# Performance work log

Hardware: AMD Instinct MI355X
Metric: run time of the kernel (lower is better)

Reference implementation:

```python
import jax, jax.numpy as jnp
import numpy as np

B, C, N = 16, 256, 2048  # C = channels_m, inputs have C//2 channels
C2 = C // 2
BN_EPS = 1e-5


def setup_inputs() -> dict:
    key = jax.random.key(0)
    ks = jax.random.split(key, 8)
    s = 1.0 / np.sqrt(C2)
    return {
        "q": jax.random.normal(ks[0], (B, C2, N), dtype=jnp.float32),
        "x": jax.random.normal(ks[1], (B, C2, N), dtype=jnp.float32),
        "Wq": jax.random.normal(ks[2], (C2, C2), dtype=jnp.float32) * s,
        "Wk": jax.random.normal(ks[3], (C2, C2), dtype=jnp.float32) * s,
        "Wv": jax.random.normal(ks[4], (C, C2), dtype=jnp.float32) * s,
        "bv": jax.random.normal(ks[5], (C,), dtype=jnp.float32) * 0.01,
        "Wt": jax.random.normal(ks[6], (C, C), dtype=jnp.float32) * (1.0 / np.sqrt(C)),
        "bt": jax.random.normal(ks[7], (C,), dtype=jnp.float32) * 0.01,
        "gamma": jnp.ones((C,), dtype=jnp.float32),
        "beta": jnp.zeros((C,), dtype=jnp.float32),
        "running_mean": jnp.zeros((C,), dtype=jnp.float32),
        "running_var": jnp.ones((C,), dtype=jnp.float32),
    }


def reference(q, x, Wq, Wk, Wv, bv, Wt, bt, gamma, beta, running_mean, running_var):
    # 1x1 Conv1d == channel matmul. q, x: [B, C2, N]
    x_q = jnp.einsum('oc,bcn->bno', Wq, q)                     # [B, N, C2]
    x_k = jnp.einsum('oc,bcn->bon', Wk, x)                     # [B, C2, N]
    x_v = jnp.einsum('oc,bcn->bon', Wv, q) + bv[None, :, None]  # [B, C, N]

    energy = jnp.einsum('bnc,bcm->bnm', x_q, x_k)              # [B, N, N]
    attn = jax.nn.softmax(energy, axis=-1)
    # extra column-wise L1 renormalization (offset-attention)
    attn = attn / (1e-9 + attn.sum(axis=1, keepdims=True))

    x_r = jnp.einsum('bcn,bnm->bcm', x_v, attn)                # [B, C, N]
    x2 = jnp.einsum('oc,bcn->bon', Wv, x) + bv[None, :, None]  # v_conv(x): [B, C, N]

    t = jnp.einsum('oc,bcn->bon', Wt, x2 - x_r) + bt[None, :, None]
    inv = gamma * jax.lax.rsqrt(running_var + BN_EPS)
    bn = t * inv[None, :, None] + (beta - running_mean * inv)[None, :, None]
    return jax.nn.relu(bn) + x2
```

## Files before the change

kernel.cpp:

```cpp
#include <hip/hip_runtime.h>
#include <hip/hip_bf16.h>
#include <math.h>

#define BB 16
#define CC 256
#define C2 128
#define NN 2048

typedef __attribute__((ext_vector_type(8))) _Float16 f16x8;
typedef __attribute__((ext_vector_type(8))) short bf16x8;
typedef __attribute__((ext_vector_type(16))) float f32x16;
typedef unsigned short u16;

#define OFF_X2   ((size_t)0)
#define OFF_U16  ((size_t)16777216)
#define UOFF_XQT ((size_t)0)
#define UOFF_XKT ((size_t)4194304)
#define UOFF_XV  ((size_t)8388608)
#define OFF_RMAX ((size_t)25165824)
#define OFF_RSUM ((size_t)25198592)
#define OFF_W16  ((size_t)29458432)
#define WOFF_WQ  ((size_t)0)
#define WOFF_WK  ((size_t)16384)
#define WOFF_WV  ((size_t)32768)
#define WOFF_WT  ((size_t)65536)

__device__ __forceinline__ u16 f2h(float f) {
    union { _Float16 h; u16 u; } v; v.h = (_Float16)f;
    return v.u;
}
__device__ __forceinline__ u16 f2bf(float f) {
    union { float f; unsigned u; } v; v.f = f;
    return (u16)((v.u + 0x7fffu + ((v.u >> 16) & 1u)) >> 16);
}

__global__ __launch_bounds__(256) void prep_w(
    const float* __restrict__ Wq, const float* __restrict__ Wk,
    const float* __restrict__ Wv, const float* __restrict__ Wt,
    u16* __restrict__ w16)
{
    int i = blockIdx.x * 256 + threadIdx.x;
    float v; u16* dst; int o, c, KC;
    if (i < 16384)      { v = Wq[i]; o = i >> 7; c = i & 127; KC = 16; dst = w16; }
    else if (i < 32768) { int j = i - 16384; v = Wk[j]; o = j >> 7; c = j & 127; KC = 16; dst = w16 + 16384; }
    else if (i < 65536) { int j = i - 32768; v = Wv[j]; o = j >> 7; c = j & 127; KC = 16; dst = w16 + 32768; }
    else                { int j = i - 65536; v = Wt[j]; o = j >> 8; c = j & 255; KC = 32; dst = w16 + 65536; }
    int idx = (((o >> 5) * KC + (c >> 3)) << 8) + ((o & 31) << 3) + (c & 7);
    dst[idx] = f2h(v);
}

__global__ __launch_bounds__(256, 2) void proj_fused(
    const float* __restrict__ q, const float* __restrict__ x,
    const u16* __restrict__ wq16, const u16* __restrict__ wk16,
    const u16* __restrict__ wv16, const float* __restrict__ bias,
    u16* __restrict__ xqT, u16* __restrict__ xkT,
    u16* __restrict__ xv_bf, float* __restrict__ x2_f32)
{
    __shared__ u16 t_s[64 * 136];
    __shared__ u16 st[16384];
    int tid = threadIdx.x, lane = tid & 63, wave = tid >> 6;
    int zb = blockIdx.z, b = zb >> 1, which = zb & 1;
    int n0 = blockIdx.x * 64;
    const float* in  = which ? x : q;
    const u16*   wqk = which ? wk16 : wq16;
    u16*         outT = which ? xkT : xqT;
    {
        int r = tid >> 2;
        int nc = (tid & 3) * 16;
        #pragma unroll
        for (int hh = 0; hh < 2; ++hh) {
            const float4* ip4 = (const float4*)(in + ((size_t)b * C2 + hh * 64 + r) * NN + n0 + nc);
            #pragma unroll
            for (int jj = 0; jj < 4; ++jj) {
                float4 v = ip4[jj];
                int nbase = nc + jj * 4;
                t_s[(nbase + 0) * 136 + hh * 64 + r] = f2h(v.x);
                t_s[(nbase + 1) * 136 + hh * 64 + r] = f2h(v.y);
                t_s[(nbase + 2) * 136 + hh * 64 + r] = f2h(v.z);
                t_s[(nbase + 3) * 136 + hh * 64 + r] = f2h(v.w);
            }
        }
    }
    __syncthreads();
    int nsub = wave & 1, g = wave >> 1;
    int lrow = lane & 31, h = lane >> 5, lk8 = h * 8;
    const u16* brow = &t_s[(nsub * 32 + lrow) * 136 + lk8];
    f32x16 aq0, aq1, av0, av1, av2, av3;
    #pragma unroll
    for (int r = 0; r < 16; ++r)
        { aq0[r]=0.f; aq1[r]=0.f; av0[r]=0.f; av1[r]=0.f; av2[r]=0.f; av3[r]=0.f; }
    const u16* wqA = wqk  + (size_t)(2 * g) * 4096 + h * 256 + lrow * 8;
    const u16* wvA = wv16 + (size_t)(4 * g) * 4096 + h * 256 + lrow * 8;
    #pragma unroll
    for (int kk = 0; kk < 8; ++kk) {
        f16x8 bf = *(const f16x8*)&brow[kk * 16];
        f16x8 q0 = *(const f16x8*)&wqA[kk * 512];
        f16x8 q1 = *(const f16x8*)&wqA[4096 + kk * 512];
        aq0 = __builtin_amdgcn_mfma_f32_32x32x16_f16(bf, q0, aq0, 0, 0, 0);
        aq1 = __builtin_amdgcn_mfma_f32_32x32x16_f16(bf, q1, aq1, 0, 0, 0);
        f16x8 v0 = *(const f16x8*)&wvA[kk * 512];
        f16x8 v1 = *(const f16x8*)&wvA[4096 + kk * 512];
        f16x8 v2 = *(const f16x8*)&wvA[8192 + kk * 512];
        f16x8 v3 = *(const f16x8*)&wvA[12288 + kk * 512];
        av0 = __builtin_amdgcn_mfma_f32_32x32x16_f16(v0, bf, av0, 0, 0, 0);
        av1 = __builtin_amdgcn_mfma_f32_32x32x16_f16(v1, bf, av1, 0, 0, 0);
        av2 = __builtin_amdgcn_mfma_f32_32x32x16_f16(v2, bf, av2, 0, 0, 0);
        av3 = __builtin_amdgcn_mfma_f32_32x32x16_f16(v3, bf, av3, 0, 0, 0);
    }
    __syncthreads();
    {
        int off = (nsub * 16 + g * 8 + (lrow >> 3)) * 256 + (lrow & 7);
        #pragma unroll
        for (int r = 0; r < 16; ++r) {
            int ro = (r & 3) + 8 * (r >> 2) + 4 * h;
            t_s[off + ro * 8]        = f2h(aq0[r]);
            t_s[off + 1024 + ro * 8] = f2h(aq1[r]);
        }
    }
    if (which == 0) {
        int off = (g * 4 * 8 + nsub * 4 + (lrow >> 3)) * 256 + (lrow & 7);
        #pragma unroll
        for (int r = 0; r < 16; ++r) {
            int ro = (r & 3) + 8 * (r >> 2) + 4 * h;
            int c0r = g * 128 + ro;
            st[off + ro * 8]        = f2bf(av0[r] + bias[c0r]);
            st[off + 2048 + ro * 8] = f2bf(av1[r] + bias[c0r + 32]);
            st[off + 4096 + ro * 8] = f2bf(av2[r] + bias[c0r + 64]);
            st[off + 6144 + ro * 8] = f2bf(av3[r] + bias[c0r + 96]);
        }
    }
    __syncthreads();
    {
        u16* outb = outT + (size_t)b * NN * C2 + (size_t)(n0 >> 5) * 4096;
        for (int i = tid; i < 1024; i += 256)
            *(uint4*)&outb[i * 8] = *(uint4*)&t_s[i * 8];
    }
    if (which == 0) {
        u16* xvb = xv_bf + (size_t)b * CC * NN + (size_t)(n0 >> 3) * 256;
        for (int i = tid; i < 2048; i += 256) {
            int ct = i >> 8, j = i & 255;
            *(uint4*)&xvb[(size_t)ct * 65536 + j * 8] = *(uint4*)&st[ct * 2048 + j * 8];
        }
    } else {
        int n = n0 + nsub * 32 + lrow;
        #pragma unroll
        for (int r = 0; r < 16; ++r) {
            int ro = (r & 3) + 8 * (r >> 2) + 4 * h;
            int c0r = g * 128 + ro;
            x2_f32[((size_t)b * CC + c0r) * NN + n]      = av0[r] + bias[c0r];
            x2_f32[((size_t)b * CC + c0r + 32) * NN + n] = av1[r] + bias[c0r + 32];
            x2_f32[((size_t)b * CC + c0r + 64) * NN + n] = av2[r] + bias[c0r + 64];
            x2_f32[((size_t)b * CC + c0r + 96) * NN + n] = av3[r] + bias[c0r + 96];
        }
    }
}

__global__ __launch_bounds__(512, 4) void rowstats_mfma(
    const u16* __restrict__ xqT, const u16* __restrict__ xkT,
    float* __restrict__ rmax, float* __restrict__ rsum)
{
    __shared__ float Mp[8][32];
    __shared__ float Sp[8][32];
    const int tid  = threadIdx.x;
    int flat = blockIdx.x + gridDim.x * blockIdx.y;
    int xcd = flat & 7, rank = flat >> 3;
    const int b  = xcd * 2 + (rank >> 5);
    const int n0 = (rank & 31) * 64;
    const int lane = tid & 63;
    const int wave = tid >> 6;
    const int lrow = lane & 31;
    const int h    = lane >> 5;
    const u16* xqb = xqT + (size_t)b * NN * C2;
    const u16* xkb = xkT + (size_t)b * NN * C2;
    const int mquad = wave >> 1, nsub = wave & 1;

    f16x8 bR[8];
    {
        const u16* bp = xqb + ((size_t)((n0 >> 5) + nsub) * 16) * 256 + h * 256 + lrow * 8;
        #pragma unroll
        for (int kk = 0; kk < 8; ++kk) bR[kk] = *(const f16x8*)&bp[kk * 512];
    }
    float runM = -1e30f, runS = 0.f;
    const u16* ap = xkb + (size_t)(mquad * 16) * 256 + h * 256 + lrow * 8;
    for (int m0 = 0; m0 < NN; m0 += 128) {
        f32x16 e0;
        #pragma unroll
        for (int r = 0; r < 16; ++r) e0[r] = 0.f;
        #pragma unroll
        for (int kk = 0; kk < 8; ++kk) {
            f16x8 a0 = *(const f16x8*)&ap[kk * 512];
            e0 = __builtin_amdgcn_mfma_f32_32x32x16_f16(a0, bR[kk], e0, 0, 0, 0);
        }
        ap += 16384;
        float tm = e0[0];
        #pragma unroll
        for (int r = 1; r < 16; ++r) tm = fmaxf(tm, e0[r]);
        float newM = fmaxf(runM, tm);
        float sc = __expf(runM - newM);
        float ts = 0.f;
        #pragma unroll
        for (int r = 0; r < 16; ++r) ts += __expf(e0[r] - newM);
        runS = runS * sc + ts;
        runM = newM;
    }
    float oM = __shfl_xor(runM, 32, 64);
    float oS = __shfl_xor(runS, 32, 64);
    float M2 = fmaxf(runM, oM);
    float S2 = runS * __expf(runM - M2) + oS * __expf(oM - M2);
    if (lane < 32) { Mp[wave][lane] = M2; Sp[wave][lane] = S2; }
    __syncthreads();
    if (tid < 64) {
        int ns = tid >> 5, li = tid & 31;
        float Ma = Mp[ns][li],     Mb = Mp[ns + 2][li];
        float Mc = Mp[ns + 4][li], Md = Mp[ns + 6][li];
        float Mf = fmaxf(fmaxf(Ma, Mb), fmaxf(Mc, Md));
        float Sf = Sp[ns][li]     * __expf(Ma - Mf) + Sp[ns + 2][li] * __expf(Mb - Mf)
                 + Sp[ns + 4][li] * __expf(Mc - Mf) + Sp[ns + 6][li] * __expf(Md - Mf);
        rmax[(size_t)b * NN + n0 + tid] = Mf;
        rsum[(size_t)b * NN + n0 + tid] = Sf;
    }
}

__global__ __launch_bounds__(512, 4) void pv_mfma(
    const u16* __restrict__ xqT, const u16* __restrict__ xkT,
    const u16* __restrict__ xv, const float* __restrict__ rmax,
    const float* __restrict__ rsum, const float* __restrict__ x2,
    const u16* __restrict__ wt16, const float* __restrict__ bt,
    const float* __restrict__ gamma, const float* __restrict__ beta,
    const float* __restrict__ rmean, const float* __restrict__ rvar,
    float* __restrict__ out)
{
    __shared__ __align__(16) u16 smem[19584];
    const int tid = threadIdx.x;
    int flat = blockIdx.x + gridDim.x * blockIdx.y;
    int xcd = flat & 7, rank = flat >> 3;
    const int b  = xcd * 2 + (rank >> 5);
    const int m0 = (rank & 31) * 64;
    const int lane = tid & 63;
    const int wave = tid >> 6;
    const int lrow = lane & 31;
    const int h    = lane >> 5;
    const int lk8  = h * 8;
    const u16* xqb = xqT + (size_t)b * NN * C2;
    const u16* xkb = xkT + (size_t)b * NN * C2;
    const u16* xvb = xv  + (size_t)b * CC * NN;
    const float* rmx = rmax + (size_t)b * NN;
    const float* rsm = rsum + (size_t)b * NN;

    if (tid < 256) {
        float iv = gamma[tid] * rsqrtf(rvar[tid] + 1e-5f);
        float* bn = (float*)(smem + 18560);
        bn[tid]       = iv;
        bn[256 + tid] = bt[tid] * iv + beta[tid] - rmean[tid] * iv;
    }

    f16x8 aK[8];
    {
        const u16* kp = xkb + ((size_t)((m0 >> 5) + (wave & 1)) * 16) * 256 + h * 256 + lrow * 8;
        #pragma unroll
        for (int kk = 0; kk < 8; ++kk) aK[kk] = *(const f16x8*)&kp[kk * 512];
    }
    const int nq = wave >> 1;
    const int nl = nq * 32 + lrow;
    const int mbase = (wave & 1) * 32 + 4 * h;
    const u16* bqbase = xqb + (size_t)nq * 4096 + h * 256 + lrow * 8;
    const u16* avbase = xvb + (size_t)wave * 65536 + h * 256 + lrow * 8;

    f32x16 acc00, acc01;
    #pragma unroll
    for (int r = 0; r < 16; ++r) { acc00[r] = 0.f; acc01[r] = 0.f; }
    float s_reg = 0.f;
    __syncthreads();

    for (int ph = 0; ph <= 16; ++ph) {
        f16x8 bq[8];
        float Mn = 0.f, Sn = 1.f;
        if (ph < 16) {
            const u16* bqp = bqbase + (size_t)ph * 16384;
            #pragma unroll
            for (int kk = 0; kk < 8; ++kk) bq[kk] = *(const f16x8*)&bqp[kk * 512];
            Mn = rmx[ph * 128 + nl];
            Sn = rsm[ph * 128 + nl];
        }
        if (ph >= 1) {
            const int t = ph - 1;
            const u16* p_prev = smem + (t & 1) * 8704;
            const u16* avp = avbase + (size_t)t * 4096;
            {
                const uint4* prp = (const uint4*)&p_prev[(tid & 63) * 136 + (tid >> 6) * 16];
                uint4 v0 = prp[0], v1 = prp[1];
                unsigned wsv[8] = {v0.x, v0.y, v0.z, v0.w, v1.x, v1.y, v1.z, v1.w};
                float ss = 0.f;
                #pragma unroll
                for (int j = 0; j < 8; ++j) {
                    union { unsigned u; float f; } lo, hi;
                    lo.u = wsv[j] << 16;
                    hi.u = wsv[j] & 0xffff0000u;
                    ss += lo.f + hi.f;
                }
                s_reg += ss;
            }
            const u16* br0 = &p_prev[lrow * 136 + lk8];
            const u16* br1 = &p_prev[(32 + lrow) * 136 + lk8];
            __builtin_amdgcn_s_setprio(1);
            #pragma unroll
            for (int kk = 0; kk < 8; ++kk) {
                bf16x8 a0 = *(const bf16x8*)&avp[kk * 512];
                bf16x8 b0 = *(const bf16x8*)&br0[kk * 16];
                bf16x8 b1 = *(const bf16x8*)&br1[kk * 16];
                acc00 = __builtin_amdgcn_mfma_f32_32x32x16_bf16(a0, b0, acc00, 0, 0, 0);
                acc01 = __builtin_amdgcn_mfma_f32_32x32x16_bf16(a0, b1, acc01, 0, 0, 0);
            }
            __builtin_amdgcn_s_setprio(0);
        }
        if (ph < 16) {
            f32x16 e0;
            #pragma unroll
            for (int r = 0; r < 16; ++r) e0[r] = 0.f;
            __builtin_amdgcn_s_setprio(1);
            #pragma unroll
            for (int kk = 0; kk < 8; ++kk)
                e0 = __builtin_amdgcn_mfma_f32_32x32x16_f16(aK[kk], bq[kk], e0, 0, 0, 0);
            __builtin_amdgcn_s_setprio(0);
            float Si = 1.f / Sn;
            u16* p_cur = smem + (ph & 1) * 8704;
            #pragma unroll
            for (int r = 0; r < 16; ++r) {
                int ml = mbase + (r & 3) + 8 * (r >> 2);
                p_cur[ml * 136 + nl] = f2bf(__expf(e0[r] - Mn) * Si);
            }
        }
        __syncthreads();
    }
    float* s_part = (float*)(smem + 17408);
    s_part[(tid & 63) * 8 + (tid >> 6)] = s_reg;
    __syncthreads();
    float* sinv = (float*)(smem + 18432);
    if (tid < 64) {
        float ss = 0.f;
        #pragma unroll
        for (int j = 0; j < 8; ++j) ss += s_part[tid * 8 + j];
        sinv[tid] = 1.f / (1e-9f + ss);
    }
    __syncthreads();
    u16* dts = smem;
    const float* x2b = x2 + (size_t)b * CC * NN;
    float si0 = sinv[lrow], si1 = sinv[32 + lrow];
    #pragma unroll
    for (int r = 0; r < 16; ++r) {
        int ro = (r & 3) + 8 * (r >> 2) + 4 * h;
        int c = wave * 32 + ro;
        float d0 = x2b[(size_t)c * NN + m0 + lrow]      - acc00[r] * si0;
        float d1 = x2b[(size_t)c * NN + m0 + 32 + lrow] - acc01[r] * si1;
        dts[lrow * 264 + c]        = f2h(d0);
        dts[(32 + lrow) * 264 + c] = f2h(d1);
    }
    __syncthreads();
    {
        float* inv_s = (float*)(smem + 18560);
        float* add_s = inv_s + 256;
        int rt0 = (wave >> 1) * 2;
        int ns2 = wave & 1;
        const u16* brow2 = &dts[(ns2 * 32 + lrow) * 264 + lk8];
        const u16* a0p = wt16 + (size_t)rt0 * 8192 + h * 256 + lrow * 8;
        const u16* a1p = a0p + 8192;
        f32x16 o0a, o1a;
        #pragma unroll
        for (int r = 0; r < 16; ++r) { o0a[r] = 0.f; o1a[r] = 0.f; }
        #pragma unroll
        for (int kk = 0; kk < 16; ++kk) {
            f16x8 bb2 = *(const f16x8*)&brow2[kk * 16];
            f16x8 a0 = *(const f16x8*)&a0p[kk * 512];
            f16x8 a1 = *(const f16x8*)&a1p[kk * 512];
            o0a = __builtin_amdgcn_mfma_f32_32x32x16_f16(a0, bb2, o0a, 0, 0, 0);
            o1a = __builtin_amdgcn_mfma_f32_32x32x16_f16(a1, bb2, o1a, 0, 0, 0);
        }
        int n = m0 + ns2 * 32 + lrow;
        float* outb = out + (size_t)b * CC * NN;
        #pragma unroll
        for (int r = 0; r < 16; ++r) {
            int ro = (r & 3) + 8 * (r >> 2) + 4 * h;
            int ol0 = rt0 * 32 + ro, ol1 = ol0 + 32;
            float t0 = o0a[r] * inv_s[ol0] + add_s[ol0];
            float t1 = o1a[r] * inv_s[ol1] + add_s[ol1];
            outb[(size_t)ol0 * NN + n] = fmaxf(t0, 0.f) + x2b[(size_t)ol0 * NN + n];
            outb[(size_t)ol1 * NN + n] = fmaxf(t1, 0.f) + x2b[(size_t)ol1 * NN + n];
        }
    }
}

extern "C" void kernel_launch(void* const* d_in, const int* in_sizes, int n_in,
                              void* d_out, int out_size, void* d_ws, size_t ws_size,
                              hipStream_t stream)
{
    const float* q     = (const float*)d_in[0];
    const float* x     = (const float*)d_in[1];
    const float* Wq    = (const float*)d_in[2];
    const float* Wk    = (const float*)d_in[3];
    const float* Wv    = (const float*)d_in[4];
    const float* bv    = (const float*)d_in[5];
    const float* Wt    = (const float*)d_in[6];
    const float* bt    = (const float*)d_in[7];
    const float* gamma = (const float*)d_in[8];
    const float* beta  = (const float*)d_in[9];
    const float* rmean = (const float*)d_in[10];
    const float* rvar  = (const float*)d_in[11];
    float* out = (float*)d_out;
    float* ws  = (float*)d_ws;

    float* x2   = ws + OFF_X2;
    u16*   u1   = (u16*)(ws + OFF_U16);
    u16*   xqT  = u1 + UOFF_XQT;
    u16*   xkT  = u1 + UOFF_XKT;
    u16*   xv   = u1 + UOFF_XV;
    float* rmax = ws + OFF_RMAX;
    float* rsum = ws + OFF_RSUM;
    u16*   w16  = (u16*)(ws + OFF_W16);

    dim3 blk(256);
    prep_w<<<dim3(512), blk, 0, stream>>>(Wq, Wk, Wv, Wt, w16);
    proj_fused<<<dim3(NN/64, 1, 2*BB), blk, 0, stream>>>(
        q, x, w16 + WOFF_WQ, w16 + WOFF_WK, w16 + WOFF_WV, bv,
        xqT, xkT, xv, x2);
    rowstats_mfma<<<dim3(NN/64, BB), dim3(512), 0, stream>>>(xqT, xkT, rmax, rsum);
    pv_mfma<<<dim3(NN/64, BB), dim3(512), 0, stream>>>(
        xqT, xkT, xv, rmax, rsum, x2, w16 + WOFF_WT, bt, gamma, beta,
        rmean, rvar, out);
}
```

Before: 249.7 us.

## Drop weight prep kernel, convert fp32 weights inline; widen proj to 512 threads

Removes the separate prep_w launch that converted and tiled weights to fp16, and instead loads fp32 weights directly in the projection and output-transform MFMA loops, converting them to fp16 in registers. The projection kernel is also restructured to 512 threads per block with fewer accumulators per wave and a smaller staging buffer, writing xv in two staged passes. This saves one kernel launch and its global round trip. In exchange, each block reads fp32 weights at twice the bytes with strided row access and repeats the conversion work.

```diff
diff --git a/kernel.cpp b/kernel.cpp
--- a/kernel.cpp
+++ b/kernel.cpp
@@ -19,11 +19,6 @@
 #define UOFF_XV  ((size_t)8388608)
 #define OFF_RMAX ((size_t)25165824)
 #define OFF_RSUM ((size_t)25198592)
-#define OFF_W16  ((size_t)29458432)
-#define WOFF_WQ  ((size_t)0)
-#define WOFF_WK  ((size_t)16384)
-#define WOFF_WV  ((size_t)32768)
-#define WOFF_WT  ((size_t)65536)
 
 __device__ __forceinline__ u16 f2h(float f) {
     union { _Float16 h; u16 u; } v; v.h = (_Float16)f;
@@ -33,124 +28,112 @@
     union { float f; unsigned u; } v; v.f = f;
     return (u16)((v.u + 0x7fffu + ((v.u >> 16) & 1u)) >> 16);
 }
-
-__global__ __launch_bounds__(256) void prep_w(
+__device__ __forceinline__ f16x8 cvt8(const float* __restrict__ p) {
+    float4 a = *(const float4*)p;
+    float4 b = *(const float4*)(p + 4);
+    f16x8 r;
+    r[0] = (_Float16)a.x; r[1] = (_Float16)a.y;
+    r[2] = (_Float16)a.z; r[3] = (_Float16)a.w;
+    r[4] = (_Float16)b.x; r[5] = (_Float16)b.y;
+    r[6] = (_Float16)b.z; r[7] = (_Float16)b.w;
+    return r;
+}
+
+__global__ __launch_bounds__(512, 4) void proj_fused(
+    const float* __restrict__ q, const float* __restrict__ x,
     const float* __restrict__ Wq, const float* __restrict__ Wk,
-    const float* __restrict__ Wv, const float* __restrict__ Wt,
-    u16* __restrict__ w16)
-{
-    int i = blockIdx.x * 256 + threadIdx.x;
-    float v; u16* dst; int o, c, KC;
-    if (i < 16384)      { v = Wq[i]; o = i >> 7; c = i & 127; KC = 16; dst = w16; }
-    else if (i < 32768) { int j = i - 16384; v = Wk[j]; o = j >> 7; c = j & 127; KC = 16; dst = w16 + 16384; }
-    else if (i < 65536) { int j = i - 32768; v = Wv[j]; o = j >> 7; c = j & 127; KC = 16; dst = w16 + 32768; }
-    else                { int j = i - 65536; v = Wt[j]; o = j >> 8; c = j & 255; KC = 32; dst = w16 + 65536; }
-    int idx = (((o >> 5) * KC + (c >> 3)) << 8) + ((o & 31) << 3) + (c & 7);
-    dst[idx] = f2h(v);
-}
-
-__global__ __launch_bounds__(256, 2) void proj_fused(
-    const float* __restrict__ q, const float* __restrict__ x,
-    const u16* __restrict__ wq16, const u16* __restrict__ wk16,
-    const u16* __restrict__ wv16, const float* __restrict__ bias,
+    const float* __restrict__ Wv, const float* __restrict__ bias,
     u16* __restrict__ xqT, u16* __restrict__ xkT,
     u16* __restrict__ xv_bf, float* __restrict__ x2_f32)
 {
     __shared__ u16 t_s[64 * 136];
-    __shared__ u16 st[16384];
+    __shared__ u16 stg[8192];
     int tid = threadIdx.x, lane = tid & 63, wave = tid >> 6;
     int zb = blockIdx.z, b = zb >> 1, which = zb & 1;
     int n0 = blockIdx.x * 64;
     const float* in  = which ? x : q;
-    const u16*   wqk = which ? wk16 : wq16;
+    const float* wqk = which ? Wk : Wq;
     u16*         outT = which ? xkT : xqT;
     {
-        int r = tid >> 2;
-        int nc = (tid & 3) * 16;
-        #pragma unroll
-        for (int hh = 0; hh < 2; ++hh) {
-            const float4* ip4 = (const float4*)(in + ((size_t)b * C2 + hh * 64 + r) * NN + n0 + nc);
-            #pragma unroll
-            for (int jj = 0; jj < 4; ++jj) {
-                float4 v = ip4[jj];
-                int nbase = nc + jj * 4;
-                t_s[(nbase + 0) * 136 + hh * 64 + r] = f2h(v.x);
-                t_s[(nbase + 1) * 136 + hh * 64 + r] = f2h(v.y);
-                t_s[(nbase + 2) * 136 + hh * 64 + r] = f2h(v.z);
-                t_s[(nbase + 3) * 136 + hh * 64 + r] = f2h(v.w);
-            }
-        }
-    }
-    __syncthreads();
-    int nsub = wave & 1, g = wave >> 1;
+        int c  = tid >> 2;
+        int qn = (tid & 3) * 16;
+        const float4* ip4 = (const float4*)(in + ((size_t)b * C2 + c) * NN + n0 + qn);
+        #pragma unroll
+        for (int jj = 0; jj < 4; ++jj) {
+            float4 v = ip4[jj];
+            int nb = qn + jj * 4;
+            t_s[(nb + 0) * 136 + c] = f2h(v.x);
+            t_s[(nb + 1) * 136 + c] = f2h(v.y);
+            t_s[(nb + 2) * 136 + c] = f2h(v.z);
+            t_s[(nb + 3) * 136 + c] = f2h(v.w);
+        }
+    }
+    __syncthreads();
+    int nsub = wave & 1, gp = wave >> 1;
     int lrow = lane & 31, h = lane >> 5, lk8 = h * 8;
     const u16* brow = &t_s[(nsub * 32 + lrow) * 136 + lk8];
-    f32x16 aq0, aq1, av0, av1, av2, av3;
+    f32x16 aq0, av0, av1;
     #pragma unroll
-    for (int r = 0; r < 16; ++r)
-        { aq0[r]=0.f; aq1[r]=0.f; av0[r]=0.f; av1[r]=0.f; av2[r]=0.f; av3[r]=0.f; }
-    const u16* wqA = wqk  + (size_t)(2 * g) * 4096 + h * 256 + lrow * 8;
-    const u16* wvA = wv16 + (size_t)(4 * g) * 4096 + h * 256 + lrow * 8;
+    for (int r = 0; r < 16; ++r) { aq0[r] = 0.f; av0[r] = 0.f; av1[r] = 0.f; }
+    const float* wqA  = wqk + (size_t)(gp * 32 + lrow) * C2 + h * 8;
+    const float* wvA0 = Wv  + (size_t)(gp * 64 + lrow) * C2 + h * 8;
+    const float* wvA1 = Wv  + (size_t)(gp * 64 + 32 + lrow) * C2 + h * 8;
     #pragma unroll
     for (int kk = 0; kk < 8; ++kk) {
         f16x8 bf = *(const f16x8*)&brow[kk * 16];
-        f16x8 q0 = *(const f16x8*)&wqA[kk * 512];
-        f16x8 q1 = *(const f16x8*)&wqA[4096 + kk * 512];
+        f16x8 q0 = cvt8(&wqA[kk * 16]);
         aq0 = __builtin_amdgcn_mfma_f32_32x32x16_f16(bf, q0, aq0, 0, 0, 0);
-        aq1 = __builtin_amdgcn_mfma_f32_32x32x16_f16(bf, q1, aq1, 0, 0, 0);
-        f16x8 v0 = *(const f16x8*)&wvA[kk * 512];
-        f16x8 v1 = *(const f16x8*)&wvA[4096 + kk * 512];
-        f16x8 v2 = *(const f16x8*)&wvA[8192 + kk * 512];
-        f16x8 v3 = *(const f16x8*)&wvA[12288 + kk * 512];
+        f16x8 v0 = cvt8(&wvA0[kk * 16]);
+        f16x8 v1 = cvt8(&wvA1[kk * 16]);
         av0 = __builtin_amdgcn_mfma_f32_32x32x16_f16(v0, bf, av0, 0, 0, 0);
         av1 = __builtin_amdgcn_mfma_f32_32x32x16_f16(v1, bf, av1, 0, 0, 0);
-        av2 = __builtin_amdgcn_mfma_f32_32x32x16_f16(v2, bf, av2, 0, 0, 0);
-        av3 = __builtin_amdgcn_mfma_f32_32x32x16_f16(v3, bf, av3, 0, 0, 0);
-    }
-    __syncthreads();
-    {
-        int off = (nsub * 16 + g * 8 + (lrow >> 3)) * 256 + (lrow & 7);
+    }
+    {
+        int off = (nsub * 16 + gp * 4 + (lrow >> 3)) * 256 + (lrow & 7);
         #pragma unroll
         for (int r = 0; r < 16; ++r) {
             int ro = (r & 3) + 8 * (r >> 2) + 4 * h;
-            t_s[off + ro * 8]        = f2h(aq0[r]);
-            t_s[off + 1024 + ro * 8] = f2h(aq1[r]);
-        }
+            stg[off + ro * 8] = f2h(aq0[r]);
+        }
+    }
+    __syncthreads();
+    {
+        u16* outb = outT + (size_t)b * NN * C2 + (size_t)(n0 >> 5) * 4096;
+        for (int i = tid; i < 1024; i += 512)
+            *(uint4*)&outb[i * 8] = *(uint4*)&stg[i * 8];
     }
     if (which == 0) {
-        int off = (g * 4 * 8 + nsub * 4 + (lrow >> 3)) * 256 + (lrow & 7);
+        #pragma unroll
+        for (int ct2 = 0; ct2 < 2; ++ct2) {
+            __syncthreads();
+            if ((gp >> 1) == ct2) {
+                int off = (((gp & 1) * 2) * 8 + nsub * 4 + (lrow >> 3)) * 256 + (lrow & 7);
+                #pragma unroll
+                for (int r = 0; r < 16; ++r) {
+                    int ro = (r & 3) + 8 * (r >> 2) + 4 * h;
+                    int c0 = gp * 64 + ro;
+                    stg[off + ro * 8]        = f2bf(av0[r] + bias[c0]);
+                    stg[off + 2048 + ro * 8] = f2bf(av1[r] + bias[c0 + 32]);
+                }
+            }
+            __syncthreads();
+            u16* xvb = xv_bf + (size_t)b * CC * NN + (size_t)(ct2 * 4) * 65536
+                             + (size_t)(n0 >> 3) * 256;
+            for (int i = tid; i < 1024; i += 512) {
+                int ctile = i >> 8;
+                int m8 = (i & 255) * 8;
+                *(uint4*)&xvb[(size_t)ctile * 65536 + m8] = *(uint4*)&stg[ctile * 2048 + m8];
+            }
+        }
+    } else {
+        float* x2b = x2_f32 + (size_t)b * CC * NN;
+        int n = n0 + nsub * 32 + lrow;
         #pragma unroll
         for (int r = 0; r < 16; ++r) {
             int ro = (r & 3) + 8 * (r >> 2) + 4 * h;
-            int c0r = g * 128 + ro;
-            st[off + ro * 8]        = f2bf(av0[r] + bias[c0r]);
-            st[off + 2048 + ro * 8] = f2bf(av1[r] + bias[c0r + 32]);
-            st[off + 4096 + ro * 8] = f2bf(av2[r] + bias[c0r + 64]);
-            st[off + 6144 + ro * 8] = f2bf(av3[r] + bias[c0r + 96]);
-        }
-    }
-    __syncthreads();
-    {
-        u16* outb = outT + (size_t)b * NN * C2 + (size_t)(n0 >> 5) * 4096;
-        for (int i = tid; i < 1024; i += 256)
-            *(uint4*)&outb[i * 8] = *(uint4*)&t_s[i * 8];
-    }
-    if (which == 0) {
-        u16* xvb = xv_bf + (size_t)b * CC * NN + (size_t)(n0 >> 3) * 256;
-        for (int i = tid; i < 2048; i += 256) {
-            int ct = i >> 8, j = i & 255;
-            *(uint4*)&xvb[(size_t)ct * 65536 + j * 8] = *(uint4*)&st[ct * 2048 + j * 8];
-        }
-    } else {
-        int n = n0 + nsub * 32 + lrow;
-        #pragma unroll
-        for (int r = 0; r < 16; ++r) {
-            int ro = (r & 3) + 8 * (r >> 2) + 4 * h;
-            int c0r = g * 128 + ro;
-            x2_f32[((size_t)b * CC + c0r) * NN + n]      = av0[r] + bias[c0r];
-            x2_f32[((size_t)b * CC + c0r + 32) * NN + n] = av1[r] + bias[c0r + 32];
-            x2_f32[((size_t)b * CC + c0r + 64) * NN + n] = av2[r] + bias[c0r + 64];
-            x2_f32[((size_t)b * CC + c0r + 96) * NN + n] = av3[r] + bias[c0r + 96];
+            int c0 = gp * 64 + ro;
+            x2b[(size_t)c0 * NN + n]        = av0[r] + bias[c0];
+            x2b[(size_t)(c0 + 32) * NN + n] = av1[r] + bias[c0 + 32];
         }
     }
 }
@@ -225,7 +208,7 @@
     const u16* __restrict__ xqT, const u16* __restrict__ xkT,
     const u16* __restrict__ xv, const float* __restrict__ rmax,
     const float* __restrict__ rsum, const float* __restrict__ x2,
-    const u16* __restrict__ wt16, const float* __restrict__ bt,
+    const float* __restrict__ Wt, const float* __restrict__ bt,
     const float* __restrict__ gamma, const float* __restrict__ beta,
     const float* __restrict__ rmean, const float* __restrict__ rvar,
     float* __restrict__ out)
@@ -362,16 +345,16 @@
         int rt0 = (wave >> 1) * 2;
         int ns2 = wave & 1;
         const u16* brow2 = &dts[(ns2 * 32 + lrow) * 264 + lk8];
-        const u16* a0p = wt16 + (size_t)rt0 * 8192 + h * 256 + lrow * 8;
-        const u16* a1p = a0p + 8192;
+        const float* a0p = Wt + (size_t)(rt0 * 32 + lrow) * CC + h * 8;
+        const float* a1p = a0p + (size_t)32 * CC;
         f32x16 o0a, o1a;
         #pragma unroll
         for (int r = 0; r < 16; ++r) { o0a[r] = 0.f; o1a[r] = 0.f; }
         #pragma unroll
         for (int kk = 0; kk < 16; ++kk) {
             f16x8 bb2 = *(const f16x8*)&brow2[kk * 16];
-            f16x8 a0 = *(const f16x8*)&a0p[kk * 512];
-            f16x8 a1 = *(const f16x8*)&a1p[kk * 512];
+            f16x8 a0 = cvt8(&a0p[kk * 16]);
+            f16x8 a1 = cvt8(&a1p[kk * 16]);
             o0a = __builtin_amdgcn_mfma_f32_32x32x16_f16(a0, bb2, o0a, 0, 0, 0);
             o1a = __builtin_amdgcn_mfma_f32_32x32x16_f16(a1, bb2, o1a, 0, 0, 0);
         }
@@ -415,15 +398,10 @@
     u16*   xv   = u1 + UOFF_XV;
     float* rmax = ws + OFF_RMAX;
     float* rsum = ws + OFF_RSUM;
-    u16*   w16  = (u16*)(ws + OFF_W16);
-
-    dim3 blk(256);
-    prep_w<<<dim3(512), blk, 0, stream>>>(Wq, Wk, Wv, Wt, w16);
-    proj_fused<<<dim3(NN/64, 1, 2*BB), blk, 0, stream>>>(
-        q, x, w16 + WOFF_WQ, w16 + WOFF_WK, w16 + WOFF_WV, bv,
-        xqT, xkT, xv, x2);
+
+    proj_fused<<<dim3(NN/64, 1, 2*BB), dim3(512), 0, stream>>>(
+        q, x, Wq, Wk, Wv, bv, xqT, xkT, xv, x2);
     rowstats_mfma<<<dim3(NN/64, BB), dim3(512), 0, stream>>>(xqT, xkT, rmax, rsum);
     pv_mfma<<<dim3(NN/64, BB), dim3(512), 0, stream>>>(
-        xqT, xkT, xv, rmax, rsum, x2, w16 + WOFF_WT, bt, gamma, beta,
-        rmean, rvar, out);
-}
+        xqT, xkT, xv, rmax, rsum, x2, Wt, bt, gamma, beta, rmean, rvar, out);
+}
```

Measured after the change: 322.8 us. 29.3% more time.
